# Optimization experiments

Measured on AMD Instinct MI355X. Metric: run time of the kernel, lower is better.

Reference implementation:

```python
import jax, jax.numpy as jnp
import numpy as np

N_AUTHOR, N_PAPER, N_FIELD, N_INST = 100000, 200000, 50000, 8000
IN_F, OUT_F, N_REL = 128, 64, 7


def setup_inputs() -> dict:
    key = jax.random.key(0)
    ks = jax.random.split(key, 24)
    d = {}
    d['x_author'] = jax.random.normal(ks[0], (N_AUTHOR, IN_F), jnp.float32)
    d['x_field_of_study'] = jax.random.normal(ks[1], (N_FIELD, IN_F), jnp.float32)
    d['x_institution'] = jax.random.normal(ks[2], (N_INST, IN_F), jnp.float32)
    d['x_paper'] = jax.random.normal(ks[3], (N_PAPER, IN_F), jnp.float32)
    # params (xavier-ish scale)
    d['weight'] = jax.random.normal(ks[4], (N_REL, IN_F, OUT_F), jnp.float32) * 0.05
    d['self_loop_weight'] = jax.random.normal(ks[5], (IN_F, OUT_F), jnp.float32) * 0.05
    d['bias'] = jnp.zeros((OUT_F,), jnp.float32)
    # edge lists: (name, n_edges, n_src, n_dst)
    rels = [('writes', 1000000, N_AUTHOR, N_PAPER),
            ('rev_writes', 1000000, N_PAPER, N_AUTHOR),
            ('cites', 1000000, N_PAPER, N_PAPER),
            ('has_topic', 800000, N_PAPER, N_FIELD),
            ('rev_has_topic', 800000, N_FIELD, N_PAPER),
            ('affiliated_with', 200000, N_AUTHOR, N_INST),
            ('rev_affiliated_with', 200000, N_INST, N_AUTHOR)]
    i = 6
    for name, ne, ns, nd in rels:
        d[name + '_src'] = jax.random.randint(ks[i], (ne,), 0, ns, jnp.int32); i += 1
        d[name + '_dst'] = jax.random.randint(ks[i], (ne,), 0, nd, jnp.int32); i += 1
    return d


def _rel_conv(x_src, W, src, dst, n_dst):
    # GraphConv(norm='right', weight=W): project src feats (in>out so matmul first),
    # gather along edges, scatter-sum to dst, divide by in-degree (clamped to 1).
    msg = (x_src @ W)[src]                                   # [E, OUT_F]
    agg = jax.ops.segment_sum(msg, dst, num_segments=n_dst)  # [n_dst, OUT_F]
    deg = jax.ops.segment_sum(jnp.ones(dst.shape, msg.dtype), dst, num_segments=n_dst)
    return agg / jnp.maximum(deg, 1.0)[:, None]


def reference(x_author, x_field_of_study, x_institution, x_paper,
              weight, self_loop_weight, bias,
              writes_src, writes_dst, rev_writes_src, rev_writes_dst,
              cites_src, cites_dst, has_topic_src, has_topic_dst,
              rev_has_topic_src, rev_has_topic_dst,
              affiliated_with_src, affiliated_with_dst,
              rev_affiliated_with_src, rev_affiliated_with_dst):
    # weight index order == rel_names order
    h_paper = (_rel_conv(x_author, weight[0], writes_src, writes_dst, N_PAPER)
               + _rel_conv(x_paper, weight[2], cites_src, cites_dst, N_PAPER)
               + _rel_conv(x_field_of_study, weight[4], rev_has_topic_src, rev_has_topic_dst, N_PAPER))
    h_author = (_rel_conv(x_paper, weight[1], rev_writes_src, rev_writes_dst, N_AUTHOR)
                + _rel_conv(x_institution, weight[6], rev_affiliated_with_src, rev_affiliated_with_dst, N_AUTHOR))
    h_field = _rel_conv(x_paper, weight[3], has_topic_src, has_topic_dst, N_FIELD)
    h_inst = _rel_conv(x_author, weight[5], affiliated_with_src, affiliated_with_dst, N_INST)

    def finalize(h, x_dst):
        # self-loop matmul + bias + relu fusion
        return jax.nn.relu(h + x_dst @ self_loop_weight + bias)

    return (finalize(h_author, x_author),
            finalize(h_field, x_field_of_study),
            finalize(h_inst, x_institution),
            finalize(h_paper, x_paper))
```

## Files before the change

kernel.cpp:

```cpp
#include <hip/hip_runtime.h>
#include <hip/hip_bf16.h>

#define IN_F 128
#define OUT_F 64

typedef __hip_bfloat16 bf16;
typedef __attribute__((ext_vector_type(8))) short short8;
typedef __attribute__((ext_vector_type(4))) float f32x4;

#define N_AUTHOR 100000
#define N_PAPER  200000
#define N_FIELD  50000
#define N_INST   8000
#define N_NODES  858000
#define E_TOTAL  5000000

#define OUT_AUTHOR 0L
#define OUT_FIELD  (6400000L)
#define OUT_INST   (9600000L)
#define OUT_PAPER  (10112000L)

#define DG_WRITES   0
#define DG_RWRITES  200000
#define DG_CITES    300000
#define DG_HTOPIC   500000
#define DG_RHTOPIC  550000
#define DG_AFFIL    750000
#define DG_RAFFIL   758000

#define YR_WRITES   0L
#define YR_RWRITES  100000L
#define YR_CITES    300000L
#define YR_HTOPIC   500000L
#define YR_RHTOPIC  700000L
#define YR_AFFIL    750000L
#define YR_RAFFIL   850000L

__device__ inline short f2bf(float f) {
    __hip_bfloat16 h = __float2bfloat16(f);
    return __builtin_bit_cast(short, h);
}
__device__ inline float bflo(unsigned u) {
    unsigned v = u << 16;
    return __builtin_bit_cast(float, v);
}
__device__ inline float bfhi(unsigned u) {
    unsigned v = u & 0xFFFF0000u;
    return __builtin_bit_cast(float, v);
}

__device__ __forceinline__ void degSegS(const int* __restrict__ dst, int E,
                                        int* __restrict__ deg, int chunk,
                                        int lo, int wid) {
    const int base = chunk * 2048 + (int)threadIdx.x * 4;
    #pragma unroll
    for (int it = 0; it < 2; it++) {
        int i = base + it * 1024;
        if (i + 3 < E) {
            int4 d = *(const int4*)(dst + i);
            if ((unsigned)(d.x - lo) < (unsigned)wid) atomicAdd(&deg[d.x], 1);
            if ((unsigned)(d.y - lo) < (unsigned)wid) atomicAdd(&deg[d.y], 1);
            if ((unsigned)(d.z - lo) < (unsigned)wid) atomicAdd(&deg[d.z], 1);
            if ((unsigned)(d.w - lo) < (unsigned)wid) atomicAdd(&deg[d.w], 1);
        } else {
            for (int k = 0; k < 4; k++) {
                int ii = i + k;
                if (ii < E) {
                    int dd = dst[ii];
                    if ((unsigned)(dd - lo) < (unsigned)wid) atomicAdd(&deg[dd], 1);
                }
            }
        }
    }
}

__global__ __launch_bounds__(256) void deg_all(
    const int* d0, const int* d1, const int* d2, const int* d3,
    const int* d4, const int* d5, const int* d6, int* __restrict__ deg) {
    const int b = blockIdx.x;
    const int s = b & 7;
    const int t = b >> 3;
    if      (t < 489)  degSegS(d0, 1000000, deg + DG_WRITES,  t,        s * 25000, 25000);
    else if (t < 978)  degSegS(d1, 1000000, deg + DG_RWRITES, t - 489,  s * 12500, 12500);
    else if (t < 1467) degSegS(d2, 1000000, deg + DG_CITES,   t - 978,  s * 25000, 25000);
    else if (t < 1858) degSegS(d3,  800000, deg + DG_HTOPIC,  t - 1467, s * 6250,  6250);
    else if (t < 2249) degSegS(d4,  800000, deg + DG_RHTOPIC, t - 1858, s * 25000, 25000);
    else if (t < 2347) degSegS(d5,  200000, deg + DG_AFFIL,   t - 2249, s * 1000,  1000);
    else               degSegS(d6,  200000, deg + DG_RAFFIL,  t - 2347, s * 12500, 12500);
}

__global__ __launch_bounds__(256) void scan1(const int* __restrict__ deg,
                                             int* __restrict__ off,
                                             int* __restrict__ bsums, int n) {
    __shared__ int ts[256];
    const int tid = threadIdx.x;
    const int base = blockIdx.x * 1024 + tid * 4;
    int4 v = {0, 0, 0, 0};
    if (base < n) v = *(const int4*)(deg + base);
    int sum = v.x + v.y + v.z + v.w;
    ts[tid] = sum;
    __syncthreads();
    for (int o = 1; o < 256; o <<= 1) {
        int t = (tid >= o) ? ts[tid - o] : 0;
        __syncthreads();
        ts[tid] += t;
        __syncthreads();
    }
    int pre = ts[tid] - sum;
    if (base < n) {
        int4 e;
        e.x = pre;
        e.y = pre + v.x;
        e.z = pre + v.x + v.y;
        e.w = pre + v.x + v.y + v.z;
        *(int4*)(off + base) = e;
    }
    if (tid == 255) bsums[blockIdx.x] = ts[255];
}

__global__ __launch_bounds__(1024) void scan2(int* __restrict__ bsums, int nb) {
    __shared__ int ts[1024];
    const int tid = threadIdx.x;
    int v = (tid < nb) ? bsums[tid] : 0;
    ts[tid] = v;
    __syncthreads();
    for (int o = 1; o < 1024; o <<= 1) {
        int t = (tid >= o) ? ts[tid - o] : 0;
        __syncthreads();
        ts[tid] += t;
        __syncthreads();
    }
    if (tid < nb) bsums[tid] = ts[tid] - v;
}

__global__ __launch_bounds__(256) void scan3(int* __restrict__ off,
                                             int* __restrict__ cursor,
                                             const int* __restrict__ bsums,
                                             int n, int e_total) {
    const int tid = threadIdx.x;
    const int base = blockIdx.x * 1024 + tid * 4;
    const int bp = bsums[blockIdx.x];
    if (base < n) {
        int4 v = *(const int4*)(off + base);
        v.x += bp; v.y += bp; v.z += bp; v.w += bp;
        *(int4*)(off + base) = v;
        *(int4*)(cursor + base) = v;
    }
    if (blockIdx.x == 0 && tid == 0) off[n] = e_total;
}

__device__ __forceinline__ void fillSegS(const int* __restrict__ src,
                                         const int* __restrict__ dst, int E,
                                         int* __restrict__ cursor,
                                         int* __restrict__ csr, int chunk,
                                         int lo, int wid) {
    const int base = chunk * 2048 + (int)threadIdx.x * 4;
    #pragma unroll
    for (int it = 0; it < 2; it++) {
        int i = base + it * 1024;
        if (i + 3 < E) {
            int4 d = *(const int4*)(dst + i);
            int4 sv = *(const int4*)(src + i);
            if ((unsigned)(d.x - lo) < (unsigned)wid) { int p = atomicAdd(&cursor[d.x], 1); csr[p] = sv.x; }
            if ((unsigned)(d.y - lo) < (unsigned)wid) { int p = atomicAdd(&cursor[d.y], 1); csr[p] = sv.y; }
            if ((unsigned)(d.z - lo) < (unsigned)wid) { int p = atomicAdd(&cursor[d.z], 1); csr[p] = sv.z; }
            if ((unsigned)(d.w - lo) < (unsigned)wid) { int p = atomicAdd(&cursor[d.w], 1); csr[p] = sv.w; }
        } else {
            for (int k = 0; k < 4; k++) {
                int ii = i + k;
                if (ii < E) {
                    int dd = dst[ii];
                    if ((unsigned)(dd - lo) < (unsigned)wid) {
                        int p = atomicAdd(&cursor[dd], 1);
                        csr[p] = src[ii];
                    }
                }
            }
        }
    }
}

__global__ __launch_bounds__(256) void fill_all(
    const int* s0, const int* d0, const int* s1, const int* d1,
    const int* s2, const int* d2, const int* s3, const int* d3,
    const int* s4, const int* d4, const int* s5, const int* d5,
    const int* s6, const int* d6,
    int* __restrict__ cursor, int* __restrict__ csr) {
    const int b = blockIdx.x;
    const int s = b & 7;
    const int t = b >> 3;
    if      (t < 489)  fillSegS(s0, d0, 1000000, cursor + DG_WRITES,  csr, t,        s * 25000, 25000);
    else if (t < 978)  fillSegS(s1, d1, 1000000, cursor + DG_RWRITES, csr, t - 489,  s * 12500, 12500);
    else if (t < 1467) fillSegS(s2, d2, 1000000, cursor + DG_CITES,   csr, t - 978,  s * 25000, 25000);
    else if (t < 1858) fillSegS(s3, d3,  800000, cursor + DG_HTOPIC,  csr, t - 1467, s * 6250,  6250);
    else if (t < 2249) fillSegS(s4, d4,  800000, cursor + DG_RHTOPIC, csr, t - 1858, s * 25000, 25000);
    else if (t < 2347) fillSegS(s5, d5,  200000, cursor + DG_AFFIL,   csr, t - 2249, s * 1000,  1000);
    else               fillSegS(s6, d6,  200000, cursor + DG_RAFFIL,  csr, t - 2347, s * 12500, 12500);
}

__global__ __launch_bounds__(256) void prep_wt(const float* __restrict__ W7,
                                               const float* __restrict__ slw,
                                               short* __restrict__ Wt) {
    const int mat = blockIdx.x;
    const float* Ws = (mat < 7) ? (W7 + (size_t)mat * IN_F * OUT_F) : slw;
    short* Wo = Wt + (size_t)mat * IN_F * OUT_F;
    for (int i = threadIdx.x; i < IN_F * OUT_F; i += 256) {
        int n = i >> 7;
        int k = i & 127;
        Wo[i] = f2bf(Ws[k * OUT_F + n]);
    }
}

template <int R>
__device__ __forceinline__ void projBody(
    int blk, const float* __restrict__ X,
    const short* __restrict__ wt0, const short* __restrict__ wt1,
    const short* __restrict__ wt2, const short* __restrict__ wtS,
    const float* __restrict__ bias,
    bf16* __restrict__ Y0, bf16* __restrict__ Y1, bf16* __restrict__ Y2,
    float* __restrict__ OutSelf) {
    const int tid = threadIdx.x;
    const int wave = tid >> 6;
    const int lane = tid & 63;
    const int m = lane & 15;
    const int quad = lane >> 4;
    const int rowBase = blk * 16;
    const int ncol = wave * 16 + m;

    short8 af[4];
    const float* xrow = X + (size_t)(rowBase + m) * IN_F + quad * 8;
    #pragma unroll
    for (int kb = 0; kb < 4; kb++) {
        float4 x0 = *(const float4*)(xrow + kb * 32);
        float4 x1 = *(const float4*)(xrow + kb * 32 + 4);
        short8 a;
        a[0] = f2bf(x0.x); a[1] = f2bf(x0.y); a[2] = f2bf(x0.z); a[3] = f2bf(x0.w);
        a[4] = f2bf(x1.x); a[5] = f2bf(x1.y); a[6] = f2bf(x1.z); a[7] = f2bf(x1.w);
        af[kb] = a;
    }

    const short* wts[3] = {wt0, wt1, wt2};
    bf16* Ys[3] = {Y0, Y1, Y2};

    #pragma unroll
    for (int r = 0; r < R; r++) {
        const short* wrow = wts[r] + (size_t)ncol * IN_F + quad * 8;
        f32x4 acc = {0.f, 0.f, 0.f, 0.f};
        #pragma unroll
        for (int kb = 0; kb < 4; kb++) {
            short8 bfr = *(const short8*)(wrow + kb * 32);
            acc = __builtin_amdgcn_mfma_f32_16x16x32_bf16(af[kb], bfr, acc, 0, 0, 0);
        }
        bf16* Yr = Ys[r];
        #pragma unroll
        for (int reg = 0; reg < 4; reg++) {
            int row = rowBase + quad * 4 + reg;
            Yr[(size_t)row * OUT_F + ncol] = __float2bfloat16(acc[reg]);
        }
    }

    {
        const short* wrow = wtS + (size_t)ncol * IN_F + quad * 8;
        f32x4 acc = {0.f, 0.f, 0.f, 0.f};
        #pragma unroll
        for (int kb = 0; kb < 4; kb++) {
            short8 bfr = *(const short8*)(wrow + kb * 32);
            acc = __builtin_amdgcn_mfma_f32_16x16x32_bf16(af[kb], bfr, acc, 0, 0, 0);
        }
        const float b = bias[ncol];
        #pragma unroll
        for (int reg = 0; reg < 4; reg++) {
            int row = rowBase + quad * 4 + reg;
            OutSelf[(size_t)row * OUT_F + ncol] = acc[reg] + b;
        }
    }
}

__global__ __launch_bounds__(256) void proj_all(
    const float* __restrict__ x_author, const float* __restrict__ x_field,
    const float* __restrict__ x_inst,   const float* __restrict__ x_paper,
    const short* __restrict__ wt, const float* __restrict__ bias,
    bf16* __restrict__ y, float* __restrict__ out) {
    int b = blockIdx.x;
    if (b < 12500) {
        projBody<3>(b, x_paper, wt + 1 * 8192, wt + 2 * 8192, wt + 3 * 8192, wt + 7 * 8192,
                    bias, y + YR_RWRITES * OUT_F, y + YR_CITES * OUT_F, y + YR_HTOPIC * OUT_F,
                    out + OUT_PAPER);
    } else if (b < 18750) {
        projBody<2>(b - 12500, x_author, wt + 0 * 8192, wt + 5 * 8192, nullptr, wt + 7 * 8192,
                    bias, y + YR_WRITES * OUT_F, y + YR_AFFIL * OUT_F, nullptr,
                    out + OUT_AUTHOR);
    } else if (b < 21875) {
        projBody<1>(b - 18750, x_field, wt + 4 * 8192, nullptr, nullptr, wt + 7 * 8192,
                    bias, y + YR_RHTOPIC * OUT_F, nullptr, nullptr,
                    out + OUT_FIELD);
    } else {
        projBody<1>(b - 21875, x_inst, wt + 6 * 8192, nullptr, nullptr, wt + 7 * 8192,
                    bias, y + YR_RAFFIL * OUT_F, nullptr, nullptr,
                    out + OUT_INST);
    }
}

template <int NR>
__device__ __forceinline__ void gatherNode(
    int n, int lane, const int* __restrict__ csr,
    const int* __restrict__ off0, const uint4* __restrict__ y0,
    const int* __restrict__ off1, const uint4* __restrict__ y1,
    const int* __restrict__ off2, const uint4* __restrict__ y2,
    float* __restrict__ out) {
    const int g = lane >> 3;
    const int f = lane & 7;
    const int* offs[3] = {off0, off1, off2};
    const uint4* ys[3] = {y0, y1, y2};
    float acc[8] = {0.f, 0.f, 0.f, 0.f, 0.f, 0.f, 0.f, 0.f};
    #pragma unroll
    for (int r = 0; r < NR; r++) {
        const int s = offs[r][n];
        const int e = offs[r][n + 1];
        const uint4* __restrict__ yr = ys[r];
        float racc[8] = {0.f, 0.f, 0.f, 0.f, 0.f, 0.f, 0.f, 0.f};
        for (int j = s; j < e; j += 16) {
            int i0 = j + g;
            int i1 = j + 8 + g;
            int c0 = csr[min(i0, e - 1)];
            int c1 = csr[min(i1, e - 1)];
            uint4 u0 = yr[(size_t)c0 * 8 + f];
            uint4 u1 = yr[(size_t)c1 * 8 + f];
            float m0 = (i0 < e) ? 1.f : 0.f;
            float m1 = (i1 < e) ? 1.f : 0.f;
            racc[0] += m0 * bflo(u0.x); racc[1] += m0 * bfhi(u0.x);
            racc[2] += m0 * bflo(u0.y); racc[3] += m0 * bfhi(u0.y);
            racc[4] += m0 * bflo(u0.z); racc[5] += m0 * bfhi(u0.z);
            racc[6] += m0 * bflo(u0.w); racc[7] += m0 * bfhi(u0.w);
            racc[0] += m1 * bflo(u1.x); racc[1] += m1 * bfhi(u1.x);
            racc[2] += m1 * bflo(u1.y); racc[3] += m1 * bfhi(u1.y);
            racc[4] += m1 * bflo(u1.z); racc[5] += m1 * bfhi(u1.z);
            racc[6] += m1 * bflo(u1.w); racc[7] += m1 * bfhi(u1.w);
        }
        int dg = e - s;
        float inv = 1.0f / (float)(dg > 1 ? dg : 1);
        #pragma unroll
        for (int k = 0; k < 8; k++) acc[k] += racc[k] * inv;
    }
    #pragma unroll
    for (int d = 8; d <= 32; d <<= 1) {
        #pragma unroll
        for (int k = 0; k < 8; k++) acc[k] += __shfl_xor(acc[k], d, 64);
    }
    if (lane < 8) {
        float* orow = out + (size_t)n * OUT_F + f * 8;
        float4 c0 = *(float4*)orow;
        float4 c1 = *(float4*)(orow + 4);
        c0.x = fmaxf(c0.x + acc[0], 0.f); c0.y = fmaxf(c0.y + acc[1], 0.f);
        c0.z = fmaxf(c0.z + acc[2], 0.f); c0.w = fmaxf(c0.w + acc[3], 0.f);
        c1.x = fmaxf(c1.x + acc[4], 0.f); c1.y = fmaxf(c1.y + acc[5], 0.f);
        c1.z = fmaxf(c1.z + acc[6], 0.f); c1.w = fmaxf(c1.w + acc[7], 0.f);
        *(float4*)orow = c0;
        *(float4*)(orow + 4) = c1;
    }
}

__global__ __launch_bounds__(256) void gather_all(
    const int* __restrict__ csr, const int* __restrict__ off,
    const bf16* __restrict__ y, float* __restrict__ out) {
    const int b = blockIdx.x;
    const int tid = threadIdx.x;
    const int lane = tid & 63;
    const int wv = tid >> 6;
    if (b < 50000) {
        gatherNode<3>(b * 4 + wv, lane, csr,
                      off + DG_WRITES,  (const uint4*)(y + YR_WRITES * OUT_F),
                      off + DG_CITES,   (const uint4*)(y + YR_CITES * OUT_F),
                      off + DG_RHTOPIC, (const uint4*)(y + YR_RHTOPIC * OUT_F),
                      out + OUT_PAPER);
    } else if (b < 75000) {
        gatherNode<2>((b - 50000) * 4 + wv, lane, csr,
                      off + DG_RWRITES, (const uint4*)(y + YR_RWRITES * OUT_F),
                      off + DG_RAFFIL,  (const uint4*)(y + YR_RAFFIL * OUT_F),
                      nullptr, nullptr,
                      out + OUT_AUTHOR);
    } else if (b < 87500) {
        gatherNode<1>((b - 75000) * 4 + wv, lane, csr,
                      off + DG_HTOPIC, (const uint4*)(y + YR_HTOPIC * OUT_F),
                      nullptr, nullptr, nullptr, nullptr,
                      out + OUT_FIELD);
    } else {
        gatherNode<1>((b - 87500) * 4 + wv, lane, csr,
                      off + DG_AFFIL, (const uint4*)(y + YR_AFFIL * OUT_F),
                      nullptr, nullptr, nullptr, nullptr,
                      out + OUT_INST);
    }
}

extern "C" void kernel_launch(void* const* d_in, const int* in_sizes, int n_in,
                              void* d_out, int out_size, void* d_ws, size_t ws_size,
                              hipStream_t stream) {
    (void)in_sizes; (void)n_in; (void)ws_size; (void)out_size;

    const float* x_author = (const float*)d_in[0];
    const float* x_field  = (const float*)d_in[1];
    const float* x_inst   = (const float*)d_in[2];
    const float* x_paper  = (const float*)d_in[3];
    const float* weight   = (const float*)d_in[4];
    const float* slw      = (const float*)d_in[5];
    const float* bias     = (const float*)d_in[6];
    float* out = (float*)d_out;

    char* w = (char*)d_ws;
    auto alignup = [](size_t v) { return (v + 127) & ~(size_t)127; };
    bf16* y  = (bf16*)w;              size_t o1 = alignup((size_t)N_NODES * OUT_F * sizeof(bf16));
    int* deg = (int*)(w + o1);        size_t o2 = o1 + alignup((size_t)N_NODES * sizeof(int));
    int* off = (int*)(w + o2);        size_t o3 = o2 + alignup(((size_t)N_NODES + 4) * sizeof(int));
    int* cursor = (int*)(w + o3);     size_t o4 = o3 + alignup((size_t)N_NODES * sizeof(int));
    int* csr = (int*)(w + o4);        size_t o5 = o4 + alignup((size_t)E_TOTAL * sizeof(int));
    int* bsums = (int*)(w + o5);      size_t o6 = o5 + alignup(2048 * sizeof(int));
    short* wt = (short*)(w + o6);

    const int* ws_p[7] = {(const int*)d_in[7],  (const int*)d_in[9],  (const int*)d_in[11],
                          (const int*)d_in[13], (const int*)d_in[15], (const int*)d_in[17],
                          (const int*)d_in[19]};
    const int* wd_p[7] = {(const int*)d_in[8],  (const int*)d_in[10], (const int*)d_in[12],
                          (const int*)d_in[14], (const int*)d_in[16], (const int*)d_in[18],
                          (const int*)d_in[20]};

    const int NBLK = (N_NODES + 1023) / 1024;
    const int SLICE_BLKS = 8 * 2445;

    prep_wt<<<8, 256, 0, stream>>>(weight, slw, wt);

    hipMemsetAsync(deg, 0, (size_t)N_NODES * sizeof(int), stream);
    deg_all<<<SLICE_BLKS, 256, 0, stream>>>(wd_p[0], wd_p[1], wd_p[2], wd_p[3],
                                            wd_p[4], wd_p[5], wd_p[6], deg);

    scan1<<<NBLK, 256, 0, stream>>>(deg, off, bsums, N_NODES);
    scan2<<<1, 1024, 0, stream>>>(bsums, NBLK);
    scan3<<<NBLK, 256, 0, stream>>>(off, cursor, bsums, N_NODES, E_TOTAL);

    fill_all<<<SLICE_BLKS, 256, 0, stream>>>(ws_p[0], wd_p[0], ws_p[1], wd_p[1],
                                             ws_p[2], wd_p[2], ws_p[3], wd_p[3],
                                             ws_p[4], wd_p[4], ws_p[5], wd_p[5],
                                             ws_p[6], wd_p[6], cursor, csr);

    proj_all<<<22375, 256, 0, stream>>>(x_author, x_field, x_inst, x_paper,
                                        wt, bias, y, out);

    gather_all<<<89500, 256, 0, stream>>>(csr, off, y, out);
}
```

Before: 1.108 ms.

## Give each projection wave its own row tile and simplify gather loop addressing

The projection kernel now gives each wave a separate 16-row tile and has it compute all four 16-column output blocks. Each X row is read and converted to bf16 once instead of four times, and the grid shrinks about fourfold, with bounds checks added for the partial last tile. The gather loop now handles 8 edges per iteration instead of 16 and uses 32-bit byte-offset addressing and a hardware reciprocal. That cuts address arithmetic but lowers the number of loads in flight per iteration, which could hurt latency hiding in this bandwidth-bound gather.

```diff
diff --git a/kernel.cpp b/kernel.cpp
--- a/kernel.cpp
+++ b/kernel.cpp
@@ -213,7 +213,7 @@
 
 template <int R>
 __device__ __forceinline__ void projBody(
-    int blk, const float* __restrict__ X,
+    int blk, int nrows, const float* __restrict__ X,
     const short* __restrict__ wt0, const short* __restrict__ wt1,
     const short* __restrict__ wt2, const short* __restrict__ wtS,
     const float* __restrict__ bias,
@@ -224,11 +224,15 @@
     const int lane = tid & 63;
     const int m = lane & 15;
     const int quad = lane >> 4;
-    const int rowBase = blk * 16;
-    const int ncol = wave * 16 + m;
+    const int rowBase = blk * 64 + wave * 16;
+    if (rowBase >= nrows) return;
+    const bool full = (rowBase + 16 <= nrows);
+
+    int arow = rowBase + m;
+    if (arow > nrows - 1) arow = nrows - 1;
 
     short8 af[4];
-    const float* xrow = X + (size_t)(rowBase + m) * IN_F + quad * 8;
+    const float* xrow = X + (size_t)arow * IN_F + quad * 8;
     #pragma unroll
     for (int kb = 0; kb < 4; kb++) {
         float4 x0 = *(const float4*)(xrow + kb * 32);
@@ -244,22 +248,37 @@
 
     #pragma unroll
     for (int r = 0; r < R; r++) {
-        const short* wrow = wts[r] + (size_t)ncol * IN_F + quad * 8;
-        f32x4 acc = {0.f, 0.f, 0.f, 0.f};
-        #pragma unroll
-        for (int kb = 0; kb < 4; kb++) {
-            short8 bfr = *(const short8*)(wrow + kb * 32);
-            acc = __builtin_amdgcn_mfma_f32_16x16x32_bf16(af[kb], bfr, acc, 0, 0, 0);
-        }
         bf16* Yr = Ys[r];
         #pragma unroll
-        for (int reg = 0; reg < 4; reg++) {
-            int row = rowBase + quad * 4 + reg;
-            Yr[(size_t)row * OUT_F + ncol] = __float2bfloat16(acc[reg]);
-        }
-    }
-
-    {
+        for (int cb = 0; cb < 4; cb++) {
+            const int ncol = cb * 16 + m;
+            const short* wrow = wts[r] + (size_t)ncol * IN_F + quad * 8;
+            f32x4 acc = {0.f, 0.f, 0.f, 0.f};
+            #pragma unroll
+            for (int kb = 0; kb < 4; kb++) {
+                short8 bfr = *(const short8*)(wrow + kb * 32);
+                acc = __builtin_amdgcn_mfma_f32_16x16x32_bf16(af[kb], bfr, acc, 0, 0, 0);
+            }
+            if (full) {
+                #pragma unroll
+                for (int reg = 0; reg < 4; reg++) {
+                    int row = rowBase + quad * 4 + reg;
+                    Yr[(size_t)row * OUT_F + ncol] = __float2bfloat16(acc[reg]);
+                }
+            } else {
+                #pragma unroll
+                for (int reg = 0; reg < 4; reg++) {
+                    int row = rowBase + quad * 4 + reg;
+                    if (row < nrows)
+                        Yr[(size_t)row * OUT_F + ncol] = __float2bfloat16(acc[reg]);
+                }
+            }
+        }
+    }
+
+    #pragma unroll
+    for (int cb = 0; cb < 4; cb++) {
+        const int ncol = cb * 16 + m;
         const short* wrow = wtS + (size_t)ncol * IN_F + quad * 8;
         f32x4 acc = {0.f, 0.f, 0.f, 0.f};
         #pragma unroll
@@ -268,10 +287,19 @@
             acc = __builtin_amdgcn_mfma_f32_16x16x32_bf16(af[kb], bfr, acc, 0, 0, 0);
         }
         const float b = bias[ncol];
-        #pragma unroll
-        for (int reg = 0; reg < 4; reg++) {
-            int row = rowBase + quad * 4 + reg;
-            OutSelf[(size_t)row * OUT_F + ncol] = acc[reg] + b;
+        if (full) {
+            #pragma unroll
+            for (int reg = 0; reg < 4; reg++) {
+                int row = rowBase + quad * 4 + reg;
+                OutSelf[(size_t)row * OUT_F + ncol] = acc[reg] + b;
+            }
+        } else {
+            #pragma unroll
+            for (int reg = 0; reg < 4; reg++) {
+                int row = rowBase + quad * 4 + reg;
+                if (row < nrows)
+                    OutSelf[(size_t)row * OUT_F + ncol] = acc[reg] + b;
+            }
         }
     }
 }
@@ -282,20 +310,20 @@
     const short* __restrict__ wt, const float* __restrict__ bias,
     bf16* __restrict__ y, float* __restrict__ out) {
     int b = blockIdx.x;
-    if (b < 12500) {
-        projBody<3>(b, x_paper, wt + 1 * 8192, wt + 2 * 8192, wt + 3 * 8192, wt + 7 * 8192,
+    if (b < 3125) {
+        projBody<3>(b, N_PAPER, x_paper, wt + 1 * 8192, wt + 2 * 8192, wt + 3 * 8192, wt + 7 * 8192,
                     bias, y + YR_RWRITES * OUT_F, y + YR_CITES * OUT_F, y + YR_HTOPIC * OUT_F,
                     out + OUT_PAPER);
-    } else if (b < 18750) {
-        projBody<2>(b - 12500, x_author, wt + 0 * 8192, wt + 5 * 8192, nullptr, wt + 7 * 8192,
+    } else if (b < 4688) {
+        projBody<2>(b - 3125, N_AUTHOR, x_author, wt + 0 * 8192, wt + 5 * 8192, nullptr, wt + 7 * 8192,
                     bias, y + YR_WRITES * OUT_F, y + YR_AFFIL * OUT_F, nullptr,
                     out + OUT_AUTHOR);
-    } else if (b < 21875) {
-        projBody<1>(b - 18750, x_field, wt + 4 * 8192, nullptr, nullptr, wt + 7 * 8192,
+    } else if (b < 5470) {
+        projBody<1>(b - 4688, N_FIELD, x_field, wt + 4 * 8192, nullptr, nullptr, wt + 7 * 8192,
                     bias, y + YR_RHTOPIC * OUT_F, nullptr, nullptr,
                     out + OUT_FIELD);
     } else {
-        projBody<1>(b - 21875, x_inst, wt + 6 * 8192, nullptr, nullptr, wt + 7 * 8192,
+        projBody<1>(b - 5470, N_INST, x_inst, wt + 6 * 8192, nullptr, nullptr, wt + 7 * 8192,
                     bias, y + YR_RAFFIL * OUT_F, nullptr, nullptr,
                     out + OUT_INST);
     }
@@ -303,42 +331,36 @@
 
 template <int NR>
 __device__ __forceinline__ void gatherNode(
-    int n, int lane, const int* __restrict__ csr,
-    const int* __restrict__ off0, const uint4* __restrict__ y0,
-    const int* __restrict__ off1, const uint4* __restrict__ y1,
-    const int* __restrict__ off2, const uint4* __restrict__ y2,
+    int n, int lane, const char* __restrict__ csrb,
+    const int* __restrict__ off0, const char* __restrict__ y0,
+    const int* __restrict__ off1, const char* __restrict__ y1,
+    const int* __restrict__ off2, const char* __restrict__ y2,
     float* __restrict__ out) {
     const int g = lane >> 3;
     const int f = lane & 7;
+    const unsigned foff = (unsigned)f << 4;
     const int* offs[3] = {off0, off1, off2};
-    const uint4* ys[3] = {y0, y1, y2};
+    const char* ys[3] = {y0, y1, y2};
     float acc[8] = {0.f, 0.f, 0.f, 0.f, 0.f, 0.f, 0.f, 0.f};
     #pragma unroll
     for (int r = 0; r < NR; r++) {
         const int s = offs[r][n];
         const int e = offs[r][n + 1];
-        const uint4* __restrict__ yr = ys[r];
+        const char* __restrict__ yb = ys[r];
         float racc[8] = {0.f, 0.f, 0.f, 0.f, 0.f, 0.f, 0.f, 0.f};
-        for (int j = s; j < e; j += 16) {
-            int i0 = j + g;
-            int i1 = j + 8 + g;
-            int c0 = csr[min(i0, e - 1)];
-            int c1 = csr[min(i1, e - 1)];
-            uint4 u0 = yr[(size_t)c0 * 8 + f];
-            uint4 u1 = yr[(size_t)c1 * 8 + f];
-            float m0 = (i0 < e) ? 1.f : 0.f;
-            float m1 = (i1 < e) ? 1.f : 0.f;
-            racc[0] += m0 * bflo(u0.x); racc[1] += m0 * bfhi(u0.x);
-            racc[2] += m0 * bflo(u0.y); racc[3] += m0 * bfhi(u0.y);
-            racc[4] += m0 * bflo(u0.z); racc[5] += m0 * bfhi(u0.z);
-            racc[6] += m0 * bflo(u0.w); racc[7] += m0 * bfhi(u0.w);
-            racc[0] += m1 * bflo(u1.x); racc[1] += m1 * bfhi(u1.x);
-            racc[2] += m1 * bflo(u1.y); racc[3] += m1 * bfhi(u1.y);
-            racc[4] += m1 * bflo(u1.z); racc[5] += m1 * bfhi(u1.z);
-            racc[6] += m1 * bflo(u1.w); racc[7] += m1 * bfhi(u1.w);
-        }
-        int dg = e - s;
-        float inv = 1.0f / (float)(dg > 1 ? dg : 1);
+        for (int j = s; j < e; j += 8) {
+            int i = j + g;
+            int ic = min(i, e - 1);
+            int c = *(const int*)(csrb + ((unsigned)ic << 2));
+            uint4 u = *(const uint4*)(yb + ((unsigned)c << 7) + foff);
+            float mk = (i < e) ? 1.f : 0.f;
+            racc[0] += mk * bflo(u.x); racc[1] += mk * bfhi(u.x);
+            racc[2] += mk * bflo(u.y); racc[3] += mk * bfhi(u.y);
+            racc[4] += mk * bflo(u.z); racc[5] += mk * bfhi(u.z);
+            racc[6] += mk * bflo(u.w); racc[7] += mk * bfhi(u.w);
+        }
+        float dg = (float)(e - s);
+        float inv = __builtin_amdgcn_rcpf(dg > 1.f ? dg : 1.f);
         #pragma unroll
         for (int k = 0; k < 8; k++) acc[k] += racc[k] * inv;
     }
@@ -367,26 +389,27 @@
     const int tid = threadIdx.x;
     const int lane = tid & 63;
     const int wv = tid >> 6;
+    const char* csrb = (const char*)csr;
     if (b < 50000) {
-        gatherNode<3>(b * 4 + wv, lane, csr,
-                      off + DG_WRITES,  (const uint4*)(y + YR_WRITES * OUT_F),
-                      off + DG_CITES,   (const uint4*)(y + YR_CITES * OUT_F),
-                      off + DG_RHTOPIC, (const uint4*)(y + YR_RHTOPIC * OUT_F),
+        gatherNode<3>(b * 4 + wv, lane, csrb,
+                      off + DG_WRITES,  (const char*)(y + YR_WRITES * OUT_F),
+                      off + DG_CITES,   (const char*)(y + YR_CITES * OUT_F),
+                      off + DG_RHTOPIC, (const char*)(y + YR_RHTOPIC * OUT_F),
                       out + OUT_PAPER);
     } else if (b < 75000) {
-        gatherNode<2>((b - 50000) * 4 + wv, lane, csr,
-                      off + DG_RWRITES, (const uint4*)(y + YR_RWRITES * OUT_F),
-                      off + DG_RAFFIL,  (const uint4*)(y + YR_RAFFIL * OUT_F),
+        gatherNode<2>((b - 50000) * 4 + wv, lane, csrb,
+                      off + DG_RWRITES, (const char*)(y + YR_RWRITES * OUT_F),
+                      off + DG_RAFFIL,  (const char*)(y + YR_RAFFIL * OUT_F),
                       nullptr, nullptr,
                       out + OUT_AUTHOR);
     } else if (b < 87500) {
-        gatherNode<1>((b - 75000) * 4 + wv, lane, csr,
-                      off + DG_HTOPIC, (const uint4*)(y + YR_HTOPIC * OUT_F),
+        gatherNode<1>((b - 75000) * 4 + wv, lane, csrb,
+                      off + DG_HTOPIC, (const char*)(y + YR_HTOPIC * OUT_F),
                       nullptr, nullptr, nullptr, nullptr,
                       out + OUT_FIELD);
     } else {
-        gatherNode<1>((b - 87500) * 4 + wv, lane, csr,
-                      off + DG_AFFIL, (const uint4*)(y + YR_AFFIL * OUT_F),
+        gatherNode<1>((b - 87500) * 4 + wv, lane, csrb,
+                      off + DG_AFFIL, (const char*)(y + YR_AFFIL * OUT_F),
                       nullptr, nullptr, nullptr, nullptr,
                       out + OUT_INST);
     }
@@ -441,8 +464,8 @@
                                              ws_p[4], wd_p[4], ws_p[5], wd_p[5],
                                              ws_p[6], wd_p[6], cursor, csr);
 
-    proj_all<<<22375, 256, 0, stream>>>(x_author, x_field, x_inst, x_paper,
-                                        wt, bias, y, out);
+    proj_all<<<5595, 256, 0, stream>>>(x_author, x_field, x_inst, x_paper,
+                                       wt, bias, y, out);
 
     gather_all<<<89500, 256, 0, stream>>>(csr, off, y, out);
 }
```

After: 1.063 ms. -4.0%, faster.
